# Optimization experiments

Hardware: AMD Instinct MI355X
Metric: run time of the kernel (lower is better)

## Reference

```python
import jax, jax.numpy as jnp
import numpy as np

N = 27          # num_classes (nodes)
C = 512         # in_channels
B = 64          # batch
EPS = 1e-5


def _bn(x, gamma, beta):
    # BatchNorm1d over [b, channels, feat]: normalize over (batch, feat), training mode (batch stats, biased var)
    mean = jnp.mean(x, axis=(0, 2), keepdims=True)
    var = jnp.mean((x - mean) ** 2, axis=(0, 2), keepdims=True)
    return gamma[None, :, None] * (x - mean) * jax.lax.rsqrt(var + EPS) + beta[None, :, None]


def _layer(x, edge, WA, WB, WE, WU, WV, ge, be, gv, bv):
    # x: [b, n, c], edge: [b, n*n, c]; edge index e = i*n + j; end[e,i]=1, start[e,j]=1
    b = x.shape[0]
    res = x
    Vix = x @ WA.T                       # [b, n, c]  (gathered to edges via end)
    Vjx = x @ WB.T                       # [b, n, c]  (gathered to edges via start)
    e_lin = edge @ WE.T                  # [b, n*n, c]
    # einsum('ev,bvc->bec', end, Vix) == broadcast Vix over j; start gathers Vjx over i
    msg = (Vix[:, :, None, :] + Vjx[:, None, :, :]).reshape(b, N * N, C) + e_lin
    edge = edge + jax.nn.relu(_bn(msg, ge, be))
    # attention: sigmoid then softmax over j (dim 2 of [b, n, n, c])
    e = jax.nn.sigmoid(edge).reshape(b, N, N, C)
    e = jax.nn.softmax(e, axis=2).reshape(b, N * N, C)
    Ujx = x @ WV.T                       # [b, n, c], gathered via start -> broadcast over i
    Ujx_e = jnp.broadcast_to(Ujx[:, None, :, :], (b, N, N, C)).reshape(b, N * N, C)
    Uix = x @ WU.T
    # einsum('ve,bec->bvc', end.T, t) == sum over j of t[b, i*n+j]
    agg = (e * Ujx_e).reshape(b, N, N, C).sum(axis=2)
    x = Uix + agg / N
    x = jax.nn.relu(res + _bn(x, gv, bv))
    return x, edge


def setup_inputs() -> dict:
    key = jax.random.key(0)
    ks = jax.random.split(key, 12)
    scale = np.sqrt(2.0 / C)
    w = lambda k: (jax.random.normal(k, (C, C), dtype=jnp.float32) * scale)
    inp = {
        "x": jax.random.normal(ks[0], (B, N, C), dtype=jnp.float32),
        "edge": jax.random.normal(ks[1], (B, N * N, C), dtype=jnp.float32),
        "WU1": w(ks[2]), "WV1": w(ks[3]), "WA1": w(ks[4]), "WB1": w(ks[5]), "WE1": w(ks[6]),
        "WU2": w(ks[7]), "WV2": w(ks[8]), "WA2": w(ks[9]), "WB2": w(ks[10]), "WE2": w(ks[11]),
        "gv1": jnp.ones((N,), jnp.float32), "bv1": jnp.zeros((N,), jnp.float32),
        "ge1": jnp.ones((N * N,), jnp.float32), "be1": jnp.zeros((N * N,), jnp.float32),
        "gv2": jnp.ones((N,), jnp.float32), "bv2": jnp.zeros((N,), jnp.float32),
        "ge2": jnp.ones((N * N,), jnp.float32), "be2": jnp.zeros((N * N,), jnp.float32),
    }
    return inp


def reference(x, edge, WU1, WV1, WA1, WB1, WE1, WU2, WV2, WA2, WB2, WE2,
              gv1, bv1, ge1, be1, gv2, bv2, ge2, be2):
    x, edge = _layer(x, edge, WA1, WB1, WE1, WU1, WV1, ge1, be1, gv1, bv1)
    x, edge = _layer(x, edge, WA2, WB2, WE2, WU2, WV2, ge2, be2, gv2, bv2)
    return x, edge
```

## Files before the change

### kernel.cpp

```cpp
#include <hip/hip_runtime.h>

typedef unsigned short u16;
typedef unsigned int u32;
typedef __bf16 bf16x8 __attribute__((ext_vector_type(8)));
typedef float f32x4 __attribute__((ext_vector_type(4)));

#define DI __device__ __forceinline__

DI u16 f2bf(float f) {
  union { float f; u32 u; } v; v.f = f;
  u32 r = (v.u + 0x7fffu + ((v.u >> 16) & 1u)) >> 16;
  return (u16)r;
}
DI float bf2f(u16 h) {
  union { u32 u; float f; } v; v.u = ((u32)h) << 16;
  return v.f;
}

constexpr float INV_M = 1.0f / 32768.0f;

__global__ void convw_k(const float* wa1, const float* wb1, const float* wu1, const float* wv1, const float* we1,
                        const float* wa2, const float* wb2, const float* wu2, const float* wv2, const float* we2,
                        u16* dst) {
  int idx = blockIdx.x * 256 + threadIdx.x;
  int m = idx >> 18;
  int i = idx & 0x3ffff;
  const float* s;
  switch (m) {
    case 0: s = wa1; break; case 1: s = wb1; break; case 2: s = wu1; break;
    case 3: s = wv1; break; case 4: s = we1; break; case 5: s = wa2; break;
    case 6: s = wb2; break; case 7: s = wu2; break; case 8: s = wv2; break;
    default: s = we2; break;
  }
  dst[idx] = f2bf(s[i]);
}

template<int EPI>
__global__ __launch_bounds__(256, 3) void gemm_k(
    const float* __restrict__ A, const u16* __restrict__ W,
    float* __restrict__ outf, int ldout,
    u16* __restrict__ msg, const float* __restrict__ V4,
    float* __restrict__ esum, float* __restrict__ esq) {
  __shared__ __align__(16) u16 lA[64 * 72];
  __shared__ __align__(16) u16 lW[256 * 72];
  const int tid = threadIdx.x;
  const int lane = tid & 63, wid = tid >> 6;
  const int wm = wid >> 1, wn = wid & 1;
  const int q = lane >> 4, l15 = lane & 15;
  const int rb = blockIdx.y, cb = blockIdx.x;

  f32x4 acc[2][8];
#pragma unroll
  for (int a = 0; a < 2; a++)
#pragma unroll
    for (int b = 0; b < 8; b++) acc[a][b] = (f32x4){0.f, 0.f, 0.f, 0.f};

  for (int k0 = 0; k0 < 512; k0 += 64) {
    __syncthreads();
#pragma unroll
    for (int t = tid; t < 512; t += 256) {
      int row = t >> 3, g = t & 7;
      const float* src = A + (((size_t)(rb * 64 + row)) << 9) + k0 + g * 8;
      float4 s0 = *(const float4*)src;
      float4 s1 = *(const float4*)(src + 4);
      uint4 p;
      p.x = f2bf(s0.x) | ((u32)f2bf(s0.y) << 16);
      p.y = f2bf(s0.z) | ((u32)f2bf(s0.w) << 16);
      p.z = f2bf(s1.x) | ((u32)f2bf(s1.y) << 16);
      p.w = f2bf(s1.z) | ((u32)f2bf(s1.w) << 16);
      *(uint4*)(lA + row * 72 + g * 8) = p;
    }
#pragma unroll
    for (int t = tid; t < 2048; t += 256) {
      int row = t >> 3, g = t & 7;
      const u16* src = W + (((size_t)(cb * 256 + row)) << 9) + k0 + g * 8;
      *(uint4*)(lW + row * 72 + g * 8) = *(const uint4*)src;
    }
    __syncthreads();
#pragma unroll
    for (int ks = 0; ks < 2; ks++) {
      const int ko = ks * 32 + q * 8;
      bf16x8 af[2], wf[8];
#pragma unroll
      for (int mt = 0; mt < 2; mt++)
        af[mt] = *(const bf16x8*)(lA + (wm * 32 + mt * 16 + l15) * 72 + ko);
#pragma unroll
      for (int nt = 0; nt < 8; nt++)
        wf[nt] = *(const bf16x8*)(lW + (wn * 128 + nt * 16 + l15) * 72 + ko);
#pragma unroll
      for (int mt = 0; mt < 2; mt++)
#pragma unroll
        for (int nt = 0; nt < 8; nt++)
          acc[mt][nt] = __builtin_amdgcn_mfma_f32_16x16x32_bf16(af[mt], wf[nt], acc[mt][nt], 0, 0, 0);
    }
  }

  if (EPI == 1) {
#pragma unroll
    for (int mt = 0; mt < 2; mt++) {
      int grow0 = rb * 64 + wm * 32 + mt * 16 + q * 4;
#pragma unroll
      for (int nt = 0; nt < 8; nt++) {
        int gcol = cb * 256 + wn * 128 + nt * 16 + l15;
#pragma unroll
        for (int r = 0; r < 4; r++)
          outf[(size_t)(grow0 + r) * ldout + gcol] = acc[mt][nt][r];
      }
    }
  } else {
    float ms[2][4], m2[2][4];
#pragma unroll
    for (int mt = 0; mt < 2; mt++) {
#pragma unroll
      for (int r = 0; r < 4; r++) {
        int grow = rb * 64 + wm * 32 + mt * 16 + q * 4 + r;
        int b = grow / 729;
        int e = grow - b * 729;
        int i = e / 27;
        int j = e - i * 27;
        const float* vix = V4 + (((size_t)(b * 27 + i)) << 11);
        const float* vjx = V4 + (((size_t)(b * 27 + j)) << 11) + 512;
        u16* mrow = msg + (((size_t)grow) << 9);
        float s1 = 0.f, s2 = 0.f;
#pragma unroll
        for (int nt = 0; nt < 8; nt++) {
          int c = cb * 256 + wn * 128 + nt * 16 + l15;
          float m = acc[mt][nt][r] + vix[c] + vjx[c];
          mrow[c] = f2bf(m);
          s1 += m;
          s2 += m * m;
        }
        ms[mt][r] = s1;
        m2[mt][r] = s2;
      }
    }
#pragma unroll
    for (int msk = 1; msk < 16; msk <<= 1) {
#pragma unroll
      for (int mt = 0; mt < 2; mt++)
#pragma unroll
        for (int r = 0; r < 4; r++) {
          ms[mt][r] += __shfl_xor(ms[mt][r], msk);
          m2[mt][r] += __shfl_xor(m2[mt][r], msk);
        }
    }
    __syncthreads();
    float* sm = (float*)lA;
    if (l15 == 0) {
#pragma unroll
      for (int mt = 0; mt < 2; mt++)
#pragma unroll
        for (int r = 0; r < 4; r++) {
          int rib = wm * 32 + mt * 16 + q * 4 + r;
          sm[wn * 64 + rib] = ms[mt][r];
          sm[128 + wn * 64 + rib] = m2[mt][r];
        }
    }
    __syncthreads();
    if (tid < 64) {
      int grow = rb * 64 + tid;
      int e = grow % 729;
      atomicAdd(&esum[e], sm[tid] + sm[64 + tid]);
      atomicAdd(&esq[e], sm[128 + tid] + sm[192 + tid]);
    }
  }
}

__global__ void eab_fin_k(const float* __restrict__ sum, const float* __restrict__ sq,
                          const float* __restrict__ g, const float* __restrict__ bt,
                          float2* __restrict__ ab, int n) {
  int i = blockIdx.x * 256 + threadIdx.x;
  if (i >= n) return;
  float mean = sum[i] * INV_M;
  float var = sq[i] * INV_M - mean * mean;
  float rs = rsqrtf(var + 1e-5f);
  float a = g[i] * rs;
  ab[i] = make_float2(a, bt[i] - mean * a);
}

__global__ __launch_bounds__(512) void edge_attn_k(
    const u16* __restrict__ msg, const float* __restrict__ ein, float* __restrict__ eout,
    const float2* __restrict__ eab, const float* __restrict__ V4,
    float* __restrict__ xnew, float* __restrict__ vsum, float* __restrict__ vsq) {
  const int bi = blockIdx.x;
  const int b = bi / 27, i = bi - b * 27;
  const int c = threadIdx.x;
  const size_t ebase = (((size_t)b * 729 + i * 27) << 9) + c;
  float texp[27];
  float ssum = 0.f;
#pragma unroll
  for (int j = 0; j < 27; j++) {
    size_t idx = ebase + (((size_t)j) << 9);
    float2 ab = eab[i * 27 + j];
    float bn = fmaf(ab.x, bf2f(msg[idx]), ab.y);
    float eo = ein[idx] + fmaxf(bn, 0.f);
    eout[idx] = eo;
    float s = 1.f / (1.f + __expf(-eo));
    float t = __expf(s);
    ssum += t;
    texp[j] = t;
  }
  float accv = 0.f;
#pragma unroll
  for (int j = 0; j < 27; j++)
    accv = fmaf(texp[j], V4[(((size_t)(b * 27 + j)) << 11) + 1536 + c], accv);
  float xn = V4[(((size_t)(b * 27 + i)) << 11) + 1024 + c] + accv / (ssum * 27.f);
  xnew[(((size_t)bi) << 9) + c] = xn;
  float v = xn, v2 = xn * xn;
#pragma unroll
  for (int m = 32; m >= 1; m >>= 1) {
    v += __shfl_xor(v, m);
    v2 += __shfl_xor(v2, m);
  }
  __shared__ float red[16];
  int w = threadIdx.x >> 6, ln = threadIdx.x & 63;
  if (ln == 0) { red[w] = v; red[8 + w] = v2; }
  __syncthreads();
  if (threadIdx.x == 0) {
    float s1 = 0.f, s2 = 0.f;
#pragma unroll
    for (int k = 0; k < 8; k++) { s1 += red[k]; s2 += red[8 + k]; }
    atomicAdd(&vsum[i], s1);
    atomicAdd(&vsq[i], s2);
  }
}

__global__ void vert_bn_k(const float* __restrict__ xnew, const float* __restrict__ res,
                          const float* __restrict__ vsum, const float* __restrict__ vsq,
                          const float* __restrict__ g, const float* __restrict__ bt,
                          float* __restrict__ out) {
  int idx = blockIdx.x * 256 + threadIdx.x;
  int i = (idx >> 9) % 27;
  float mean = vsum[i] * INV_M;
  float var = vsq[i] * INV_M - mean * mean;
  float rs = rsqrtf(var + 1e-5f);
  float a = g[i] * rs;
  float bb = bt[i] - mean * a;
  out[idx] = fmaxf(res[idx] + fmaf(a, xnew[idx], bb), 0.f);
}

extern "C" void kernel_launch(void* const* d_in, const int* in_sizes, int n_in,
                              void* d_out, int out_size, void* d_ws, size_t ws_size,
                              hipStream_t stream) {
  const float* x    = (const float*)d_in[0];
  const float* edge = (const float*)d_in[1];
  const float* WU1 = (const float*)d_in[2];
  const float* WV1 = (const float*)d_in[3];
  const float* WA1 = (const float*)d_in[4];
  const float* WB1 = (const float*)d_in[5];
  const float* WE1 = (const float*)d_in[6];
  const float* WU2 = (const float*)d_in[7];
  const float* WV2 = (const float*)d_in[8];
  const float* WA2 = (const float*)d_in[9];
  const float* WB2 = (const float*)d_in[10];
  const float* WE2 = (const float*)d_in[11];
  const float* gv1 = (const float*)d_in[12];
  const float* bv1 = (const float*)d_in[13];
  const float* ge1 = (const float*)d_in[14];
  const float* be1 = (const float*)d_in[15];
  const float* gv2 = (const float*)d_in[16];
  const float* bv2 = (const float*)d_in[17];
  const float* ge2 = (const float*)d_in[18];
  const float* be2 = (const float*)d_in[19];

  char* ws = (char*)d_ws;
  u16*   wbf  = (u16*)(ws + 0);
  float* V4   = (float*)(ws + 5242880);
  u16*   msg  = (u16*)(ws + 19398656);
  float* xnew = (float*)(ws + 67174400);
  float* x1   = (float*)(ws + 70713344);
  float* st   = (float*)(ws + 74252288);
  float* es1 = st + 0;    float* eq1 = st + 768;
  float* es2 = st + 1536; float* eq2 = st + 2304;
  float* vs1 = st + 3072; float* vq1 = st + 3104;
  float* vs2 = st + 3136; float* vq2 = st + 3168;
  float2* eab1 = (float2*)(st + 3200);
  float2* eab2 = (float2*)(st + 4672);

  float* xout = (float*)d_out;
  float* eo   = (float*)d_out + 884736;

  hipMemsetAsync(st, 0, 3200 * sizeof(float), stream);
  convw_k<<<dim3(10240), dim3(256), 0, stream>>>(WA1, WB1, WU1, WV1, WE1, WA2, WB2, WU2, WV2, WE2, wbf);

  gemm_k<1><<<dim3(8, 27), dim3(256), 0, stream>>>(x, wbf, V4, 2048, nullptr, nullptr, nullptr, nullptr);
  gemm_k<2><<<dim3(2, 729), dim3(256), 0, stream>>>(edge, wbf + 4 * 262144, nullptr, 0, msg, V4, es1, eq1);
  eab_fin_k<<<dim3(3), dim3(256), 0, stream>>>(es1, eq1, ge1, be1, eab1, 729);
  edge_attn_k<<<dim3(1728), dim3(512), 0, stream>>>(msg, edge, eo, eab1, V4, xnew, vs1, vq1);
  vert_bn_k<<<dim3(3456), dim3(256), 0, stream>>>(xnew, x, vs1, vq1, gv1, bv1, x1);

  gemm_k<1><<<dim3(8, 27), dim3(256), 0, stream>>>(x1, wbf + 5 * 262144, V4, 2048, nullptr, nullptr, nullptr, nullptr);
  gemm_k<2><<<dim3(2, 729), dim3(256), 0, stream>>>(eo, wbf + 9 * 262144, nullptr, 0, msg, V4, es2, eq2);
  eab_fin_k<<<dim3(3), dim3(256), 0, stream>>>(es2, eq2, ge2, be2, eab2, 729);
  edge_attn_k<<<dim3(1728), dim3(512), 0, stream>>>(msg, eo, eo, eab2, V4, xnew, vs2, vq2);
  vert_bn_k<<<dim3(3456), dim3(256), 0, stream>>>(xnew, x1, vs2, vq2, gv2, bv2, xout);
}
```

Measured before the change: 520.3 us.

## Store intermediate edges in bf16, use async global-to-LDS loads with swizzle, fold BN finalize

Several changes land together. The GEMM tile shrinks to 64x128 with XOR-swizzled LDS, and W (plus A when it is already bf16) is loaded via global_load_lds. The intermediate layer-1 edge output is stored as bf16 in place of msg, so layer-2's GEMM and attention read half the bytes and the fp32 edge is written only once. The BN finalize kernel is folded into edge_attn, and weight conversion is vectorized. The aim is less HBM traffic and fewer launches, at the cost of extra rounding on the intermediate edge tensor and a smaller tile with less W reuse per block.

```diff
diff --git a/kernel.cpp b/kernel.cpp
--- a/kernel.cpp
+++ b/kernel.cpp
@@ -9,12 +9,16 @@
 
 DI u16 f2bf(float f) {
   union { float f; u32 u; } v; v.f = f;
-  u32 r = (v.u + 0x7fffu + ((v.u >> 16) & 1u)) >> 16;
-  return (u16)r;
+  return (u16)((v.u + 0x7fffu + ((v.u >> 16) & 1u)) >> 16);
 }
 DI float bf2f(u16 h) {
   union { u32 u; float f; } v; v.u = ((u32)h) << 16;
   return v.f;
+}
+
+DI void gload_lds16(const void* g, void* l) {
+  __builtin_amdgcn_global_load_lds((const __attribute__((address_space(1))) u32*)g,
+                                   (__attribute__((address_space(3))) u32*)l, 16, 0, 0);
 }
 
 constexpr float INV_M = 1.0f / 32768.0f;
@@ -23,8 +27,8 @@
                         const float* wa2, const float* wb2, const float* wu2, const float* wv2, const float* we2,
                         u16* dst) {
   int idx = blockIdx.x * 256 + threadIdx.x;
-  int m = idx >> 18;
-  int i = idx & 0x3ffff;
+  int m = idx >> 16;
+  int i = (idx & 0xffff) << 2;
   const float* s;
   switch (m) {
     case 0: s = wa1; break; case 1: s = wb1; break; case 2: s = wu1; break;
@@ -32,65 +36,84 @@
     case 6: s = wb2; break; case 7: s = wu2; break; case 8: s = wv2; break;
     default: s = we2; break;
   }
-  dst[idx] = f2bf(s[i]);
-}
-
-template<int EPI>
-__global__ __launch_bounds__(256, 3) void gemm_k(
-    const float* __restrict__ A, const u16* __restrict__ W,
+  float4 v = *(const float4*)(s + i);
+  ushort4 o;
+  o.x = f2bf(v.x); o.y = f2bf(v.y); o.z = f2bf(v.z); o.w = f2bf(v.w);
+  *(ushort4*)(dst + ((size_t)m << 18) + i) = o;
+}
+
+template<int EPI, int ABF>
+__global__ __launch_bounds__(256, 5) void gemm_k(
+    const void* __restrict__ A_, const u16* __restrict__ W,
     float* __restrict__ outf, int ldout,
     u16* __restrict__ msg, const float* __restrict__ V4,
     float* __restrict__ esum, float* __restrict__ esq) {
-  __shared__ __align__(16) u16 lA[64 * 72];
-  __shared__ __align__(16) u16 lW[256 * 72];
+  __shared__ __align__(16) u16 lA[64 * 64];
+  __shared__ __align__(16) u16 lW[128 * 64];
   const int tid = threadIdx.x;
   const int lane = tid & 63, wid = tid >> 6;
   const int wm = wid >> 1, wn = wid & 1;
   const int q = lane >> 4, l15 = lane & 15;
   const int rb = blockIdx.y, cb = blockIdx.x;
-
-  f32x4 acc[2][8];
+  const int lrow8 = lane >> 3, lg = lane & 7;
+
+  f32x4 acc[2][4];
 #pragma unroll
   for (int a = 0; a < 2; a++)
 #pragma unroll
-    for (int b = 0; b < 8; b++) acc[a][b] = (f32x4){0.f, 0.f, 0.f, 0.f};
+    for (int b = 0; b < 4; b++) acc[a][b] = (f32x4){0.f, 0.f, 0.f, 0.f};
 
   for (int k0 = 0; k0 < 512; k0 += 64) {
     __syncthreads();
-#pragma unroll
-    for (int t = tid; t < 512; t += 256) {
-      int row = t >> 3, g = t & 7;
-      const float* src = A + (((size_t)(rb * 64 + row)) << 9) + k0 + g * 8;
-      float4 s0 = *(const float4*)src;
-      float4 s1 = *(const float4*)(src + 4);
-      uint4 p;
-      p.x = f2bf(s0.x) | ((u32)f2bf(s0.y) << 16);
-      p.y = f2bf(s0.z) | ((u32)f2bf(s0.w) << 16);
-      p.z = f2bf(s1.x) | ((u32)f2bf(s1.y) << 16);
-      p.w = f2bf(s1.z) | ((u32)f2bf(s1.w) << 16);
-      *(uint4*)(lA + row * 72 + g * 8) = p;
-    }
-#pragma unroll
-    for (int t = tid; t < 2048; t += 256) {
-      int row = t >> 3, g = t & 7;
-      const u16* src = W + (((size_t)(cb * 256 + row)) << 9) + k0 + g * 8;
-      *(uint4*)(lW + row * 72 + g * 8) = *(const uint4*)src;
+    if (ABF) {
+#pragma unroll
+      for (int it = 0; it < 2; it++) {
+        int ch = wid * 2 + it;
+        int row = ch * 8 + lrow8;
+        const u16* src = (const u16*)A_ + (((size_t)(rb * 64 + row)) << 9) + k0 + ((lg ^ (row & 7)) << 3);
+        gload_lds16(src, lA + ch * 512);
+      }
+    } else {
+#pragma unroll
+      for (int s = tid; s < 512; s += 256) {
+        int row = s >> 3, g = s & 7;
+        const float* src = (const float*)A_ + (((size_t)(rb * 64 + row)) << 9) + k0 + g * 8;
+        float4 s0 = *(const float4*)src;
+        float4 s1 = *(const float4*)(src + 4);
+        uint4 p;
+        p.x = f2bf(s0.x) | ((u32)f2bf(s0.y) << 16);
+        p.y = f2bf(s0.z) | ((u32)f2bf(s0.w) << 16);
+        p.z = f2bf(s1.x) | ((u32)f2bf(s1.y) << 16);
+        p.w = f2bf(s1.z) | ((u32)f2bf(s1.w) << 16);
+        *(uint4*)(lA + row * 64 + ((g ^ (row & 7)) << 3)) = p;
+      }
+    }
+#pragma unroll
+    for (int it = 0; it < 4; it++) {
+      int ch = wid * 4 + it;
+      int row = ch * 8 + lrow8;
+      const u16* src = W + (((size_t)(cb * 128 + row)) << 9) + k0 + ((lg ^ (row & 7)) << 3);
+      gload_lds16(src, lW + ch * 512);
     }
     __syncthreads();
 #pragma unroll
     for (int ks = 0; ks < 2; ks++) {
-      const int ko = ks * 32 + q * 8;
-      bf16x8 af[2], wf[8];
+      const int gk = ks * 4 + q;
+      bf16x8 af[2], wf[4];
+#pragma unroll
+      for (int mt = 0; mt < 2; mt++) {
+        int r = wm * 32 + mt * 16 + l15;
+        af[mt] = *(const bf16x8*)(lA + r * 64 + ((gk ^ (r & 7)) << 3));
+      }
+#pragma unroll
+      for (int nt = 0; nt < 4; nt++) {
+        int r = wn * 64 + nt * 16 + l15;
+        wf[nt] = *(const bf16x8*)(lW + r * 64 + ((gk ^ (r & 7)) << 3));
+      }
 #pragma unroll
       for (int mt = 0; mt < 2; mt++)
-        af[mt] = *(const bf16x8*)(lA + (wm * 32 + mt * 16 + l15) * 72 + ko);
-#pragma unroll
-      for (int nt = 0; nt < 8; nt++)
-        wf[nt] = *(const bf16x8*)(lW + (wn * 128 + nt * 16 + l15) * 72 + ko);
-#pragma unroll
-      for (int mt = 0; mt < 2; mt++)
-#pragma unroll
-        for (int nt = 0; nt < 8; nt++)
+#pragma unroll
+        for (int nt = 0; nt < 4; nt++)
           acc[mt][nt] = __builtin_amdgcn_mfma_f32_16x16x32_bf16(af[mt], wf[nt], acc[mt][nt], 0, 0, 0);
     }
   }
@@ -100,8 +123,8 @@
     for (int mt = 0; mt < 2; mt++) {
       int grow0 = rb * 64 + wm * 32 + mt * 16 + q * 4;
 #pragma unroll
-      for (int nt = 0; nt < 8; nt++) {
-        int gcol = cb * 256 + wn * 128 + nt * 16 + l15;
+      for (int nt = 0; nt < 4; nt++) {
+        int gcol = cb * 128 + wn * 64 + nt * 16 + l15;
 #pragma unroll
         for (int r = 0; r < 4; r++)
           outf[(size_t)(grow0 + r) * ldout + gcol] = acc[mt][nt][r];
@@ -123,8 +146,8 @@
         u16* mrow = msg + (((size_t)grow) << 9);
         float s1 = 0.f, s2 = 0.f;
 #pragma unroll
-        for (int nt = 0; nt < 8; nt++) {
-          int c = cb * 256 + wn * 128 + nt * 16 + l15;
+        for (int nt = 0; nt < 4; nt++) {
+          int c = cb * 128 + wn * 64 + nt * 16 + l15;
           float m = acc[mt][nt][r] + vix[c] + vjx[c];
           mrow[c] = f2bf(m);
           s1 += m;
@@ -166,35 +189,40 @@
   }
 }
 
-__global__ void eab_fin_k(const float* __restrict__ sum, const float* __restrict__ sq,
-                          const float* __restrict__ g, const float* __restrict__ bt,
-                          float2* __restrict__ ab, int n) {
-  int i = blockIdx.x * 256 + threadIdx.x;
-  if (i >= n) return;
-  float mean = sum[i] * INV_M;
-  float var = sq[i] * INV_M - mean * mean;
-  float rs = rsqrtf(var + 1e-5f);
-  float a = g[i] * rs;
-  ab[i] = make_float2(a, bt[i] - mean * a);
-}
-
+template<int INBF, int OUTBF>
 __global__ __launch_bounds__(512) void edge_attn_k(
-    const u16* __restrict__ msg, const float* __restrict__ ein, float* __restrict__ eout,
-    const float2* __restrict__ eab, const float* __restrict__ V4,
+    const u16* msg, const void* ein_, void* eout_,
+    const float* __restrict__ esum, const float* __restrict__ esq,
+    const float* __restrict__ ge, const float* __restrict__ be,
+    const float* __restrict__ V4,
     float* __restrict__ xnew, float* __restrict__ vsum, float* __restrict__ vsq) {
   const int bi = blockIdx.x;
   const int b = bi / 27, i = bi - b * 27;
   const int c = threadIdx.x;
-  const size_t ebase = (((size_t)b * 729 + i * 27) << 9) + c;
+  __shared__ float2 sab[27];
+  if (c < 27) {
+    int e = i * 27 + c;
+    float mean = esum[e] * INV_M;
+    float var = esq[e] * INV_M - mean * mean;
+    float a = ge[e] * rsqrtf(var + 1e-5f);
+    sab[c] = make_float2(a, be[e] - mean * a);
+  }
+  __syncthreads();
+  const size_t ebase = (((size_t)(b * 729 + i * 27)) << 9) + c;
+  const u16* einb = (const u16*)ein_;
+  const float* einf = (const float*)ein_;
+  u16* eoutb = (u16*)eout_;
+  float* eoutf = (float*)eout_;
   float texp[27];
   float ssum = 0.f;
 #pragma unroll
   for (int j = 0; j < 27; j++) {
     size_t idx = ebase + (((size_t)j) << 9);
-    float2 ab = eab[i * 27 + j];
+    float2 ab = sab[j];
     float bn = fmaf(ab.x, bf2f(msg[idx]), ab.y);
-    float eo = ein[idx] + fmaxf(bn, 0.f);
-    eout[idx] = eo;
+    float ei = INBF ? bf2f(einb[idx]) : einf[idx];
+    float eo = ei + fmaxf(bn, 0.f);
+    if (OUTBF) eoutb[idx] = f2bf(eo); else eoutf[idx] = eo;
     float s = 1.f / (1.f + __expf(-eo));
     float t = __expf(s);
     ssum += t;
@@ -266,32 +294,29 @@
   char* ws = (char*)d_ws;
   u16*   wbf  = (u16*)(ws + 0);
   float* V4   = (float*)(ws + 5242880);
-  u16*   msg  = (u16*)(ws + 19398656);
-  float* xnew = (float*)(ws + 67174400);
-  float* x1   = (float*)(ws + 70713344);
-  float* st   = (float*)(ws + 74252288);
-  float* es1 = st + 0;    float* eq1 = st + 768;
-  float* es2 = st + 1536; float* eq2 = st + 2304;
-  float* vs1 = st + 3072; float* vq1 = st + 3104;
-  float* vs2 = st + 3136; float* vq2 = st + 3168;
-  float2* eab1 = (float2*)(st + 3200);
-  float2* eab2 = (float2*)(st + 4672);
+  u16*   M1   = (u16*)(ws + 19398656);
+  u16*   M2   = (u16*)(ws + 67174400);
+  float* xnew = (float*)(ws + 114950144);
+  float* x1   = (float*)(ws + 118489088);
+  float* st   = (float*)(ws + 122028032);
+  float* es1 = st;         float* eq1 = st + 729;
+  float* es2 = st + 1458;  float* eq2 = st + 2187;
+  float* vs1 = st + 2916;  float* vq1 = st + 2943;
+  float* vs2 = st + 2970;  float* vq2 = st + 2997;
 
   float* xout = (float*)d_out;
   float* eo   = (float*)d_out + 884736;
 
-  hipMemsetAsync(st, 0, 3200 * sizeof(float), stream);
-  convw_k<<<dim3(10240), dim3(256), 0, stream>>>(WA1, WB1, WU1, WV1, WE1, WA2, WB2, WU2, WV2, WE2, wbf);
-
-  gemm_k<1><<<dim3(8, 27), dim3(256), 0, stream>>>(x, wbf, V4, 2048, nullptr, nullptr, nullptr, nullptr);
-  gemm_k<2><<<dim3(2, 729), dim3(256), 0, stream>>>(edge, wbf + 4 * 262144, nullptr, 0, msg, V4, es1, eq1);
-  eab_fin_k<<<dim3(3), dim3(256), 0, stream>>>(es1, eq1, ge1, be1, eab1, 729);
-  edge_attn_k<<<dim3(1728), dim3(512), 0, stream>>>(msg, edge, eo, eab1, V4, xnew, vs1, vq1);
+  hipMemsetAsync(st, 0, 3024 * sizeof(float), stream);
+  convw_k<<<dim3(2560), dim3(256), 0, stream>>>(WA1, WB1, WU1, WV1, WE1, WA2, WB2, WU2, WV2, WE2, wbf);
+
+  gemm_k<1, 0><<<dim3(16, 27), dim3(256), 0, stream>>>(x, wbf, V4, 2048, nullptr, nullptr, nullptr, nullptr);
+  gemm_k<2, 0><<<dim3(4, 729), dim3(256), 0, stream>>>(edge, wbf + 4 * 262144, nullptr, 0, M1, V4, es1, eq1);
+  edge_attn_k<0, 1><<<dim3(1728), dim3(512), 0, stream>>>(M1, edge, M1, es1, eq1, ge1, be1, V4, xnew, vs1, vq1);
   vert_bn_k<<<dim3(3456), dim3(256), 0, stream>>>(xnew, x, vs1, vq1, gv1, bv1, x1);
 
-  gemm_k<1><<<dim3(8, 27), dim3(256), 0, stream>>>(x1, wbf + 5 * 262144, V4, 2048, nullptr, nullptr, nullptr, nullptr);
-  gemm_k<2><<<dim3(2, 729), dim3(256), 0, stream>>>(eo, wbf + 9 * 262144, nullptr, 0, msg, V4, es2, eq2);
-  eab_fin_k<<<dim3(3), dim3(256), 0, stream>>>(es2, eq2, ge2, be2, eab2, 729);
-  edge_attn_k<<<dim3(1728), dim3(512), 0, stream>>>(msg, eo, eo, eab2, V4, xnew, vs2, vq2);
+  gemm_k<1, 0><<<dim3(16, 27), dim3(256), 0, stream>>>(x1, wbf + 5 * 262144, V4, 2048, nullptr, nullptr, nullptr, nullptr);
+  gemm_k<2, 1><<<dim3(4, 729), dim3(256), 0, stream>>>(M1, wbf + 9 * 262144, nullptr, 0, M2, V4, es2, eq2);
+  edge_attn_k<1, 0><<<dim3(1728), dim3(512), 0, stream>>>(M2, M1, eo, es2, eq2, ge2, be2, V4, xnew, vs2, vq2);
   vert_bn_k<<<dim3(3456), dim3(256), 0, stream>>>(xnew, x1, vs2, vq2, gv2, bv2, xout);
 }
```

After: 480.2 us. 7.7% less time.
